# Optimization experiments

Hardware: AMD Instinct MI355X
Metric: run time of the kernel (lower is better)

Reference implementation:

```python
import jax, jax.numpy as jnp
import numpy as np
import jax.lax as lax

# ---- static config (matches init_kwargs) ----
CIN, COUT = 64, 128
KS = (3, 3, 3)
STRIDE = (1, 1, 1)
PAD = (1, 1, 1)
DIL = (1, 1, 1)
RANK, ALPHA = 16, 32.0
SCALING = ALPHA / RANK
B, D, H, W = 2, 32, 32, 32
DN = ('NCDHW', 'OIDHW', 'NCDHW')


def _out_dim(L, p, d, k, s):
    return (L + 2 * p - d * (k - 1) - 1) // s + 1


def unfold3d(x, ks, stride, pad, dil):
    """x: [B,C,D,H,W] -> [B, C*kD*kH*kW, Do, Ho, Wo], channel-major (C outer, kernel offsets inner),
    matching torch unfold ordering."""
    kD, kH, kW = ks
    sD, sH, sW = stride
    pD, pH, pW = pad
    dD, dH, dW = dil
    b, c, d_, h_, w_ = x.shape
    Do = _out_dim(d_, pD, dD, kD, sD)
    Ho = _out_dim(h_, pH, dH, kH, sH)
    Wo = _out_dim(w_, pW, dW, kW, sW)
    xp = jnp.pad(x, ((0, 0), (0, 0), (pD, pD), (pH, pH), (pW, pW)))
    slices = []
    for i in range(kD):  # fixed small loop over kernel offsets (27 iters)
        for j in range(kH):
            for l in range(kW):
                sl = xp[:, :,
                        i * dD: i * dD + (Do - 1) * sD + 1: sD,
                        j * dH: j * dH + (Ho - 1) * sH + 1: sH,
                        l * dW: l * dW + (Wo - 1) * sW + 1: sW]
                slices.append(sl)
    patches = jnp.stack(slices, axis=2)  # [B, C, K, Do, Ho, Wo]
    return patches.reshape(b, c * kD * kH * kW, Do, Ho, Wo)


def fold3d_overlap_add(grid, base_spatial, ks, stride, pad, dil):
    """Depthwise conv_transpose3d with an all-ones kernel == overlap-add fold.
    grid: [B, Cout, Do, Ho, Wo] -> [B, Cout, *base_spatial]."""
    cout = grid.shape[1]
    kern = jnp.ones((cout, 1) + ks, dtype=grid.dtype)
    pads = []
    for i in range(3):
        full = dil[i] * (ks[i] - 1)
        # torch conv_transpose out = (L-1)*s - 2p + d*(k-1) + 1 + output_padding
        opad = base_spatial[i] - ((grid.shape[2 + i] - 1) * stride[i] - 2 * pad[i] + full + 1)
        pads.append((full - pad[i], full - pad[i] + opad))
    return lax.conv_general_dilated(
        grid, kern, window_strides=(1, 1, 1), padding=pads,
        lhs_dilation=stride, rhs_dilation=dil,
        dimension_numbers=DN, feature_group_count=cout)


def setup_inputs() -> dict:
    key = jax.random.key(0)
    k1, k2, k3, k4, k5 = jax.random.split(key, 5)
    in_feat = CIN * KS[0] * KS[1] * KS[2]
    x = jax.random.normal(k1, (B, CIN, D, H, W), dtype=jnp.float32)
    weight = jax.random.normal(k2, (COUT, CIN) + KS, dtype=jnp.float32) / np.sqrt(in_feat)
    bias = jax.random.normal(k3, (COUT,), dtype=jnp.float32) * 0.01
    lora_A = jax.random.normal(k4, (RANK, in_feat), dtype=jnp.float32) / np.sqrt(in_feat)
    # torch init is zeros; use small randn so LoRA branch is numerically active
    lora_B = jax.random.normal(k5, (COUT, RANK), dtype=jnp.float32) * 0.02
    return {"x": x, "weight": weight, "bias": bias, "lora_A": lora_A, "lora_B": lora_B}


def reference(x, weight, bias, lora_A, lora_B):
    # base conv3d
    base = lax.conv_general_dilated(
        x, weight, window_strides=STRIDE, padding=[(p, p) for p in PAD],
        rhs_dilation=DIL, dimension_numbers=DN)
    base = base + bias[None, :, None, None, None]
    # im2col
    cols = unfold3d(x, KS, STRIDE, PAD, DIL)              # [B, Cin*K, Do, Ho, Wo]
    # low-rank per-patch projection: cols^T @ A^T @ B^T * scaling
    low = jnp.einsum('bkdhw,rk->brdhw', cols, lora_A)      # [B, R, Do, Ho, Wo]
    lora_grid = jnp.einsum('brdhw,or->bodhw', low, lora_B) * SCALING  # [B, Cout, ...]
    # col2im overlap-add fold back to base's spatial shape
    lora_spatial = fold3d_overlap_add(lora_grid, base.shape[2:], KS, STRIDE, PAD, DIL)
    return base + lora_spatial
```

## Files before the change

### kernel.cpp

```cpp
#include <hip/hip_runtime.h>


typedef __attribute__((ext_vector_type(8))) short short8;
typedef __attribute__((ext_vector_type(4))) float float4v;

#define PV 39304
#define PH 1156

__device__ inline unsigned short f2bf(float f) {
    unsigned int u = __float_as_uint(f);
    unsigned int r = u + 0x7FFFu + ((u >> 16) & 1u);
    return (unsigned short)(r >> 16);
}

__device__ inline void gll16(const void* g, void* l) {
    __builtin_amdgcn_global_load_lds(
        (const __attribute__((address_space(1))) unsigned int*)g,
        (__attribute__((address_space(3))) unsigned int*)l, 16, 0, 0);
}

__global__ __launch_bounds__(256) void prep_kernel(const float* __restrict__ x,
                                                   const float* __restrict__ weight,
                                                   const float* __restrict__ loraA,
                                                   unsigned short* __restrict__ xt,
                                                   unsigned short* __restrict__ wpack) {
    int t = threadIdx.x;
    int blk = blockIdx.x;
    if (blk < 1024) {
        __shared__ float tile[64][65];
        int b = blk >> 9;
        int p0 = (blk & 511) * 64;
        int d = p0 >> 10;
        int h0 = (p0 >> 5) & 31;
#pragma unroll
        for (int it = 0; it < 16; ++it) {
            int idx = it * 256 + t;
            int c = idx >> 6, pp = idx & 63;
            tile[c][pp] = x[((size_t)(b * 64 + c) << 15) + p0 + pp];
        }
        __syncthreads();
#pragma unroll
        for (int it = 0; it < 8; ++it) {
            int idx = it * 256 + t;
            int pp = idx >> 5, cp = idx & 31;
            unsigned int u0 = f2bf(tile[cp * 2][pp]);
            unsigned int u1 = f2bf(tile[cp * 2 + 1][pp]);
            int h = h0 + (pp >> 5);
            int w = pp & 31;
            size_t pidx = (size_t)((b * 34 + d + 1) * 34 + h + 1) * 34 + w + 1;
            *(unsigned int*)(xt + pidx * 64 + cp * 2) = u0 | (u1 << 16);
        }
    } else if (blk < 1332) {
        int idx = (blk - 1024) * 256 + t;
        if (idx < 78608) {
            int b = idx / PV;
            int pp = idx - b * PV;
            int d = pp / PH;
            int r2 = pp - d * PH;
            int h = r2 / 34;
            int w = r2 - h * 34;
            if (d == 0 || d == 33 || h == 0 || h == 33 || w == 0 || w == 33) {
                uint4 z = {0u, 0u, 0u, 0u};
                uint4* dst = (uint4*)(xt + (size_t)idx * 64);
#pragma unroll
                for (int i = 0; i < 8; ++i) dst[i] = z;
            }
        }
    } else {
        int gid = (blk - 1332) * 256 + t;
        if (gid < 31104) {
            int frag = gid >> 6, lane = gid & 63;
            int kb = frag / 18;
            int r18 = frag - kb * 18;
            int ks = r18 / 9;
            int nf = r18 - ks * 9;
            int l16 = lane & 15, quad = lane >> 4;
            int n = nf * 16 + l16;
            int c0 = ks * 32 + quad * 8;
            unsigned int u[4];
#pragma unroll
            for (int jp = 0; jp < 4; ++jp) {
                int ca = c0 + jp * 2, cb = ca + 1;
                float v0, v1;
                if (n < 128) {
                    v0 = weight[(n * 64 + ca) * 27 + kb];
                    v1 = weight[(n * 64 + cb) * 27 + kb];
                } else {
                    v0 = loraA[(n - 128) * 1728 + ca * 27 + kb];
                    v1 = loraA[(n - 128) * 1728 + cb * 27 + kb];
                }
                u[jp] = (unsigned)f2bf(v0) | ((unsigned)f2bf(v1) << 16);
            }
            uint4 val; val.x = u[0]; val.y = u[1]; val.z = u[2]; val.w = u[3];
            *(uint4*)(wpack + (size_t)gid * 8) = val;
        }
    }
}

__global__ __launch_bounds__(256) void gemm_kernel(const unsigned short* __restrict__ xt,
                                                   const unsigned short* __restrict__ wpack,
                                                   const float* __restrict__ bias,
                                                   float* __restrict__ out,
                                                   unsigned short* __restrict__ cbuf,
                                                   float* __restrict__ low,
                                                   int use_cbuf) {
    __shared__ unsigned short Abuf[2][9216];

    int t = threadIdx.x;
    int wv = t >> 6;
    int lane = t & 63;
    int l16 = lane & 15;
    int quad = lane >> 4;

    int bid = blockIdx.x;
    int tile = ((bid & 7) << 6) | (bid >> 3);
    int b = tile >> 8;
    int d = (tile >> 3) & 31;
    int h = ((tile & 7) << 2) + wv;

    int pbase = (((b * 34 + d) * 34 + h) * 34 + l16) * 64 + quad * 8;

    float4v acc[9][2];
#pragma unroll
    for (int nf = 0; nf < 9; ++nf)
#pragma unroll
        for (int f = 0; f < 2; ++f) acc[nf][f] = (float4v){0.f, 0.f, 0.f, 0.f};

    short8 breg[2][2][2];

    auto prefA = [&](int tap, int buf) {
        const unsigned short* src = wpack + tap * 9216;
        unsigned short* dst = &Abuf[buf][0];
#pragma unroll
        for (int j = 0; j < 4; ++j) {
            int c8 = (t + j * 256) * 8;
            gll16(src + c8, dst + c8);
        }
        if (t < 128) {
            int c8 = (t + 1024) * 8;
            gll16(src + c8, dst + c8);
        }
    };
    auto loadB = [&](int tap, int buf) {
        int ki = tap / 9;
        int kjl = tap - ki * 9;
        int kj = kjl / 3;
        int kl = kjl - kj * 3;
        int koff = ki * 73984 + kj * 2176 + kl * 64;
        const unsigned short* xp = xt + pbase + koff;
        breg[buf][0][0] = *(const short8*)(xp);
        breg[buf][0][1] = *(const short8*)(xp + 1024);
        breg[buf][1][0] = *(const short8*)(xp + 32);
        breg[buf][1][1] = *(const short8*)(xp + 1056);
    };

    prefA(0, 0);
    loadB(0, 0);
    __syncthreads();

    for (int tap = 0; tap < 27; ++tap) {
        int cur = tap & 1, nxt = cur ^ 1;
        if (tap < 26) {
            prefA(tap + 1, nxt);
            loadB(tap + 1, nxt);
        }
        const unsigned short* ab = &Abuf[cur][0] + lane * 8;
#pragma unroll
        for (int ks = 0; ks < 2; ++ks) {
            short8 af[9];
#pragma unroll
            for (int nf = 0; nf < 9; ++nf)
                af[nf] = *(const short8*)(ab + (ks * 9 + nf) * 512);
#pragma unroll
            for (int nf = 0; nf < 9; ++nf) {
                acc[nf][0] = __builtin_amdgcn_mfma_f32_16x16x32_bf16(af[nf], breg[cur][ks][0], acc[nf][0], 0, 0, 0);
                acc[nf][1] = __builtin_amdgcn_mfma_f32_16x16x32_bf16(af[nf], breg[cur][ks][1], acc[nf][1], 0, 0, 0);
            }
        }
        __syncthreads();
    }

#pragma unroll
    for (int f = 0; f < 2; ++f) {
        int w = f * 16 + l16;
        int p = d * 1024 + h * 32 + w;
#pragma unroll
        for (int nf = 0; nf < 9; ++nf) {
#pragma unroll
            for (int r = 0; r < 4; ++r) {
                int o = nf * 16 + quad * 4 + r;
                float v = acc[nf][f][r];
                if (o < 128) {
                    float c = v + bias[o];
                    if (use_cbuf) cbuf[((size_t)(b * 128 + o) << 15) + p] = f2bf(c);
                    else          out[((size_t)(b * 128 + o) << 15) + p] = c;
                } else {
                    low[((size_t)(b * 16 + (o - 128)) << 15) + p] = v;
                }
            }
        }
    }
}

__global__ __launch_bounds__(256) void foldmix_kernel(const float* __restrict__ low,
                                                      const float* __restrict__ loraB,
                                                      const unsigned short* __restrict__ cbuf,
                                                      float* __restrict__ out,
                                                      int use_cbuf) {
    __shared__ float fl[16][128];
    __shared__ float lB[2048];
    int t = threadIdx.x;
    for (int i = t; i < 2048; i += 256) lB[i] = loraB[i];

    int P0 = blockIdx.x * 128;
    int b = P0 >> 15;
    int p0 = P0 & 32767;

    {
        int pair = t & 63;
        int rg = t >> 6;
        int p = p0 + pair * 2;
        int dd0 = p >> 10, hh = (p >> 5) & 31, w0 = p & 31;
        float s[4][2];
#pragma unroll
        for (int r = 0; r < 4; ++r) { s[r][0] = 0.f; s[r][1] = 0.f; }
        const float* bb = low + ((size_t)(b * 16 + rg * 4) << 15);
        for (int dd = -1; dd <= 1; ++dd) {
            int sd = dd0 + dd;
            if ((unsigned)sd >= 32u) continue;
            for (int dh = -1; dh <= 1; ++dh) {
                int sh = hh + dh;
                if ((unsigned)sh >= 32u) continue;
                int base = (sd << 10) + (sh << 5) + w0;
#pragma unroll
                for (int r = 0; r < 4; ++r) {
                    const float* q = bb + ((size_t)r << 15) + base;
                    float vm = (w0 > 0)  ? q[-1] : 0.f;
                    float v0 = q[0], v1 = q[1];
                    float v2 = (w0 < 30) ? q[2] : 0.f;
                    s[r][0] += vm + v0 + v1;
                    s[r][1] += v0 + v1 + v2;
                }
            }
        }
#pragma unroll
        for (int r = 0; r < 4; ++r) {
            fl[rg * 4 + r][pair * 2]     = s[r][0];
            fl[rg * 4 + r][pair * 2 + 1] = s[r][1];
        }
    }
    __syncthreads();

    int wv = t >> 6;
    int lane = t & 63;
    int pl = lane * 2;
    int p = p0 + pl;
    float2 f[16];
#pragma unroll
    for (int r = 0; r < 16; ++r) f[r] = *(const float2*)&fl[r][pl];

    int o0 = wv * 32;
#pragma unroll
    for (int oi = 0; oi < 32; ++oi) {
        int o = o0 + oi;
        float sa = 0.f, sb = 0.f;
#pragma unroll
        for (int r = 0; r < 16; ++r) {
            float lw = lB[o * 16 + r];
            sa += lw * f[r].x;
            sb += lw * f[r].y;
        }
        size_t idx = ((size_t)(b * 128 + o) << 15) + p;
        float cx, cy;
        if (use_cbuf) {
            unsigned int u = *(const unsigned int*)(cbuf + idx);
            cx = __uint_as_float(u << 16);
            cy = __uint_as_float(u & 0xffff0000u);
        } else {
            float2 c = *(const float2*)(out + idx);
            cx = c.x; cy = c.y;
        }
        float2 res;
        res.x = cx + 2.0f * sa;
        res.y = cy + 2.0f * sb;
        *(float2*)(out + idx) = res;
    }
}

extern "C" void kernel_launch(void* const* d_in, const int* in_sizes, int n_in,
                              void* d_out, int out_size, void* d_ws, size_t ws_size,
                              hipStream_t stream) {
    const float* x      = (const float*)d_in[0];
    const float* weight = (const float*)d_in[1];
    const float* bias   = (const float*)d_in[2];
    const float* loraA  = (const float*)d_in[3];
    const float* loraB  = (const float*)d_in[4];
    float* out = (float*)d_out;

    char* ws = (char*)d_ws;
    unsigned short* xt    = (unsigned short*)ws;
    unsigned short* wpack = (unsigned short*)(ws + 10061824);
    float* low            = (float*)(ws + 10559488);
    unsigned short* cbuf  = (unsigned short*)(ws + 14753792);
    int use_cbuf = (ws_size >= 31531008u) ? 1 : 0;

    hipLaunchKernelGGL(prep_kernel, dim3(1454), dim3(256), 0, stream, x, weight, loraA, xt, wpack);
    hipLaunchKernelGGL(gemm_kernel, dim3(512), dim3(256), 0, stream, xt, wpack, bias, out, cbuf, low, use_cbuf);
    hipLaunchKernelGGL(foldmix_kernel, dim3(512), dim3(256), 0, stream, low, loraB, cbuf, out, use_cbuf);
}
```

Before: 147.6 us.

## Fuse prep, GEMM and fold into one persistent kernel with grid barriers

Replaces the three-kernel pipeline with a single 512-block kernel that does the bf16 prep, the implicit-GEMM conv plus LoRA projection, and the fold/mix epilogue. Phases are separated by software grid-wide barriers built on atomics. Conv accumulators stay in registers across the barrier, which removes the cbuf round trip and two kernel launches. The cost is an extra memset plus spin-wait barriers, and correctness depends on all 512 blocks being co-resident (launch bounds 256,3).

```diff
diff --git a/kernel.cpp b/kernel.cpp
--- a/kernel.cpp
+++ b/kernel.cpp
@@ -6,6 +6,7 @@
 
 #define PV 39304
 #define PH 1156
+#define NBLK 512u
 
 __device__ inline unsigned short f2bf(float f) {
     unsigned int u = __float_as_uint(f);
@@ -18,6 +19,269 @@
         (const __attribute__((address_space(1))) unsigned int*)g,
         (__attribute__((address_space(3))) unsigned int*)l, 16, 0, 0);
 }
+
+__device__ inline void grid_barrier(unsigned int* bar, int slot) {
+    __syncthreads();
+    if (threadIdx.x == 0) {
+        __threadfence();
+        unsigned int* c = bar + slot * 32;
+        atomicAdd(c, 1u);
+        while (__hip_atomic_load(c, __ATOMIC_ACQUIRE, __HIP_MEMORY_SCOPE_AGENT) < NBLK) {
+            __builtin_amdgcn_s_sleep(2);
+        }
+    }
+    __syncthreads();
+    __threadfence();
+}
+
+__global__ __launch_bounds__(256, 3) void fused_kernel(
+    const float* __restrict__ x, const float* __restrict__ weight,
+    const float* __restrict__ bias, const float* __restrict__ loraA,
+    const float* __restrict__ loraB, float* __restrict__ out,
+    unsigned short* __restrict__ xt, unsigned short* __restrict__ wpack,
+    float* __restrict__ low, unsigned int* __restrict__ bar)
+{
+    __shared__ __align__(16) char smraw[36864];
+    int t = threadIdx.x;
+    int bid = blockIdx.x;
+
+    {
+        float (*tile)[65] = (float (*)[65])smraw;
+        for (int u = bid; u < 1454; u += 512) {
+            if (u < 1024) {
+                int pb = u >> 9;
+                int p0 = (u & 511) * 64;
+                int pd = p0 >> 10;
+                int ph0 = (p0 >> 5) & 31;
+#pragma unroll
+                for (int it = 0; it < 16; ++it) {
+                    int idx = it * 256 + t;
+                    int c = idx >> 6, pp = idx & 63;
+                    tile[c][pp] = x[((size_t)(pb * 64 + c) << 15) + p0 + pp];
+                }
+                __syncthreads();
+#pragma unroll
+                for (int it = 0; it < 8; ++it) {
+                    int idx = it * 256 + t;
+                    int pp = idx >> 5, cp = idx & 31;
+                    unsigned int u0 = f2bf(tile[cp * 2][pp]);
+                    unsigned int u1 = f2bf(tile[cp * 2 + 1][pp]);
+                    int ph = ph0 + (pp >> 5);
+                    int pw = pp & 31;
+                    size_t pidx = (size_t)((pb * 34 + pd + 1) * 34 + ph + 1) * 34 + pw + 1;
+                    *(unsigned int*)(xt + pidx * 64 + cp * 2) = u0 | (u1 << 16);
+                }
+            } else if (u < 1332) {
+                int idx = (u - 1024) * 256 + t;
+                if (idx < 78608) {
+                    int pb = idx / PV;
+                    int pp = idx - pb * PV;
+                    int pd = pp / PH;
+                    int r2 = pp - pd * PH;
+                    int ph = r2 / 34;
+                    int pw = r2 - ph * 34;
+                    if (pd == 0 || pd == 33 || ph == 0 || ph == 33 || pw == 0 || pw == 33) {
+                        uint4 z = {0u, 0u, 0u, 0u};
+                        uint4* dst = (uint4*)(xt + (size_t)idx * 64);
+#pragma unroll
+                        for (int i = 0; i < 8; ++i) dst[i] = z;
+                    }
+                }
+            } else {
+                int gid = (u - 1332) * 256 + t;
+                if (gid < 31104) {
+                    int frag = gid >> 6, ln = gid & 63;
+                    int kb = frag / 18;
+                    int r18 = frag - kb * 18;
+                    int ks = r18 / 9;
+                    int nf = r18 - ks * 9;
+                    int pl16 = ln & 15, pq = ln >> 4;
+                    int n = nf * 16 + pl16;
+                    int c0 = ks * 32 + pq * 8;
+                    unsigned int uu[4];
+#pragma unroll
+                    for (int jp = 0; jp < 4; ++jp) {
+                        int ca = c0 + jp * 2, cb = ca + 1;
+                        float v0, v1;
+                        if (n < 128) {
+                            v0 = weight[(n * 64 + ca) * 27 + kb];
+                            v1 = weight[(n * 64 + cb) * 27 + kb];
+                        } else {
+                            v0 = loraA[(n - 128) * 1728 + ca * 27 + kb];
+                            v1 = loraA[(n - 128) * 1728 + cb * 27 + kb];
+                        }
+                        uu[jp] = (unsigned)f2bf(v0) | ((unsigned)f2bf(v1) << 16);
+                    }
+                    uint4 val; val.x = uu[0]; val.y = uu[1]; val.z = uu[2]; val.w = uu[3];
+                    *(uint4*)(wpack + (size_t)gid * 8) = val;
+                }
+            }
+            __syncthreads();
+        }
+    }
+
+    grid_barrier(bar, 0);
+
+    int wv = t >> 6;
+    int lane = t & 63;
+    int l16 = lane & 15;
+    int quad = lane >> 4;
+
+    int tl = ((bid & 7) << 6) | (bid >> 3);
+    int b = tl >> 8;
+    int d = (tl >> 3) & 31;
+    int hb = (tl & 7) << 2;
+    int h = hb + wv;
+
+    unsigned short (*Abuf)[9216] = (unsigned short (*)[9216])smraw;
+
+    int pbase = (((b * 34 + d) * 34 + h) * 34 + l16) * 64 + quad * 8;
+
+    float4v acc[9][2];
+#pragma unroll
+    for (int nf = 0; nf < 9; ++nf)
+#pragma unroll
+        for (int f = 0; f < 2; ++f) acc[nf][f] = (float4v){0.f, 0.f, 0.f, 0.f};
+
+    short8 breg[2][2][2];
+
+    auto prefA = [&](int tap, int buf) {
+        const unsigned short* src = wpack + tap * 9216;
+        unsigned short* dst = &Abuf[buf][0];
+#pragma unroll
+        for (int j = 0; j < 4; ++j) {
+            int c8 = (t + j * 256) * 8;
+            gll16(src + c8, dst + c8);
+        }
+        if (t < 128) {
+            int c8 = (t + 1024) * 8;
+            gll16(src + c8, dst + c8);
+        }
+    };
+    auto loadB = [&](int tap, int buf) {
+        int ki = tap / 9;
+        int kjl = tap - ki * 9;
+        int kj = kjl / 3;
+        int kl = kjl - kj * 3;
+        int koff = ki * 73984 + kj * 2176 + kl * 64;
+        const unsigned short* xp = xt + pbase + koff;
+        breg[buf][0][0] = *(const short8*)(xp);
+        breg[buf][0][1] = *(const short8*)(xp + 1024);
+        breg[buf][1][0] = *(const short8*)(xp + 32);
+        breg[buf][1][1] = *(const short8*)(xp + 1056);
+    };
+
+    prefA(0, 0);
+    loadB(0, 0);
+    __syncthreads();
+
+    for (int tap = 0; tap < 27; ++tap) {
+        int cur = tap & 1, nxt = cur ^ 1;
+        if (tap < 26) {
+            prefA(tap + 1, nxt);
+            loadB(tap + 1, nxt);
+        }
+        const unsigned short* ab = &Abuf[cur][0] + lane * 8;
+#pragma unroll
+        for (int ks = 0; ks < 2; ++ks) {
+            short8 af[9];
+#pragma unroll
+            for (int nf = 0; nf < 9; ++nf)
+                af[nf] = *(const short8*)(ab + (ks * 9 + nf) * 512);
+#pragma unroll
+            for (int nf = 0; nf < 9; ++nf) {
+                acc[nf][0] = __builtin_amdgcn_mfma_f32_16x16x32_bf16(af[nf], breg[cur][ks][0], acc[nf][0], 0, 0, 0);
+                acc[nf][1] = __builtin_amdgcn_mfma_f32_16x16x32_bf16(af[nf], breg[cur][ks][1], acc[nf][1], 0, 0, 0);
+            }
+        }
+        __syncthreads();
+    }
+
+    {
+        int p = d * 1024 + h * 32;
+#pragma unroll
+        for (int f = 0; f < 2; ++f)
+#pragma unroll
+            for (int r = 0; r < 4; ++r)
+                low[((size_t)(b * 16 + quad * 4 + r) << 15) + p + f * 16 + l16] = acc[8][f][r];
+    }
+
+    grid_barrier(bar, 1);
+
+    {
+        float* fl  = (float*)smraw;
+        float* lBp = (float*)(smraw + 8192);
+        float* bsh = (float*)(smraw + 16384);
+
+        for (int i = t; i < 2048; i += 256) {
+            int o = i & 127, rr = i >> 7;
+            lBp[rr * 128 + o] = 2.0f * loraB[o * 16 + rr];
+        }
+        if (t < 128) bsh[t] = bias[t];
+
+        {
+            int pair = t & 63, rg = t >> 6;
+            int lp = pair * 2;
+            int hh = hb + (lp >> 5);
+            int w0 = lp & 31;
+            float s0[4], s1[4];
+#pragma unroll
+            for (int r = 0; r < 4; ++r) { s0[r] = 0.f; s1[r] = 0.f; }
+            const float* bb = low + ((size_t)(b * 16 + rg * 4) << 15);
+            for (int dd = -1; dd <= 1; ++dd) {
+                int sd = d + dd;
+                if ((unsigned)sd >= 32u) continue;
+                for (int dh = -1; dh <= 1; ++dh) {
+                    int sh = hh + dh;
+                    if ((unsigned)sh >= 32u) continue;
+                    int base = (sd << 10) + (sh << 5) + w0;
+#pragma unroll
+                    for (int r = 0; r < 4; ++r) {
+                        const float* q = bb + ((size_t)r << 15) + base;
+                        float vm = (w0 > 0)  ? q[-1] : 0.f;
+                        float v0 = q[0], v1 = q[1];
+                        float v2 = (w0 < 30) ? q[2] : 0.f;
+                        s0[r] += vm + v0 + v1;
+                        s1[r] += v0 + v1 + v2;
+                    }
+                }
+            }
+#pragma unroll
+            for (int r = 0; r < 4; ++r) {
+                fl[(rg * 4 + r) * 128 + lp]     = s0[r];
+                fl[(rg * 4 + r) * 128 + lp + 1] = s1[r];
+            }
+        }
+        __syncthreads();
+
+        float fa[16], fb[16];
+        int base0 = wv * 32 + l16;
+#pragma unroll
+        for (int rr = 0; rr < 16; ++rr) {
+            fa[rr] = fl[rr * 128 + base0];
+            fb[rr] = fl[rr * 128 + base0 + 16];
+        }
+#pragma unroll
+        for (int nf = 0; nf < 8; ++nf) {
+            float4v sv0 = (float4v){0.f, 0.f, 0.f, 0.f};
+            float4v sv1 = (float4v){0.f, 0.f, 0.f, 0.f};
+#pragma unroll
+            for (int rr = 0; rr < 16; ++rr) {
+                float4v lw = *(const float4v*)&lBp[rr * 128 + nf * 16 + quad * 4];
+                sv0 += lw * fa[rr];
+                sv1 += lw * fb[rr];
+            }
+            size_t ob0 = ((size_t)(b * 128 + nf * 16 + quad * 4) << 15) + (size_t)(d * 1024 + h * 32);
+#pragma unroll
+            for (int r = 0; r < 4; ++r) {
+                float bv = bsh[nf * 16 + quad * 4 + r];
+                out[ob0 + ((size_t)r << 15) + l16]      = acc[nf][0][r] + bv + sv0[r];
+                out[ob0 + ((size_t)r << 15) + 16 + l16] = acc[nf][1][r] + bv + sv1[r];
+            }
+        }
+    }
+}
+
 
 __global__ __launch_bounds__(256) void prep_kernel(const float* __restrict__ x,
                                                    const float* __restrict__ weight,
@@ -301,10 +565,17 @@
     unsigned short* xt    = (unsigned short*)ws;
     unsigned short* wpack = (unsigned short*)(ws + 10061824);
     float* low            = (float*)(ws + 10559488);
+    unsigned int* bar     = (unsigned int*)(ws + 14753792);
     unsigned short* cbuf  = (unsigned short*)(ws + 14753792);
-    int use_cbuf = (ws_size >= 31531008u) ? 1 : 0;
-
-    hipLaunchKernelGGL(prep_kernel, dim3(1454), dim3(256), 0, stream, x, weight, loraA, xt, wpack);
-    hipLaunchKernelGGL(gemm_kernel, dim3(512), dim3(256), 0, stream, xt, wpack, bias, out, cbuf, low, use_cbuf);
-    hipLaunchKernelGGL(foldmix_kernel, dim3(512), dim3(256), 0, stream, low, loraB, cbuf, out, use_cbuf);
-}
+
+    if (ws_size >= 14754048u) {
+        hipMemsetAsync(bar, 0, 256, stream);
+        hipLaunchKernelGGL(fused_kernel, dim3(512), dim3(256), 0, stream,
+                           x, weight, bias, loraA, loraB, out, xt, wpack, low, bar);
+    } else {
+        int use_cbuf = (ws_size >= 31531008u) ? 1 : 0;
+        hipLaunchKernelGGL(prep_kernel, dim3(1454), dim3(256), 0, stream, x, weight, loraA, xt, wpack);
+        hipLaunchKernelGGL(gemm_kernel, dim3(512), dim3(256), 0, stream, xt, wpack, bias, out, cbuf, low, use_cbuf);
+        hipLaunchKernelGGL(foldmix_kernel, dim3(512), dim3(256), 0, stream, low, loraB, cbuf, out, use_cbuf);
+    }
+}
```

After: 327.2 us. 122% more time.

## Load GEMM weight fragments directly from global memory instead of LDS double buffer

Applied to the files above, without the earlier changes.

Removes the LDS double-buffered staging of packed weights (global_load_lds plus a per-tap barrier). Each wave now reads its weight fragments straight from global memory, where they should be served from L2/L1 because every block shares them. The change also drops the explicit software prefetch of B and sets launch bounds to request two blocks per CU. The risks are repeated global/L1 traffic for the weights, since all four waves load the same fragments, and exposed load latency now that nothing is prefetched.

```diff
diff --git a/kernel.cpp b/kernel.cpp
--- a/kernel.cpp
+++ b/kernel.cpp
@@ -11,12 +11,6 @@
     unsigned int u = __float_as_uint(f);
     unsigned int r = u + 0x7FFFu + ((u >> 16) & 1u);
     return (unsigned short)(r >> 16);
-}
-
-__device__ inline void gll16(const void* g, void* l) {
-    __builtin_amdgcn_global_load_lds(
-        (const __attribute__((address_space(1))) unsigned int*)g,
-        (__attribute__((address_space(3))) unsigned int*)l, 16, 0, 0);
 }
 
 __global__ __launch_bounds__(256) void prep_kernel(const float* __restrict__ x,
@@ -97,15 +91,13 @@
     }
 }
 
-__global__ __launch_bounds__(256) void gemm_kernel(const unsigned short* __restrict__ xt,
-                                                   const unsigned short* __restrict__ wpack,
-                                                   const float* __restrict__ bias,
-                                                   float* __restrict__ out,
-                                                   unsigned short* __restrict__ cbuf,
-                                                   float* __restrict__ low,
-                                                   int use_cbuf) {
-    __shared__ unsigned short Abuf[2][9216];
-
+__global__ __launch_bounds__(256, 2) void gemm_kernel(const unsigned short* __restrict__ xt,
+                                                      const unsigned short* __restrict__ wpack,
+                                                      const float* __restrict__ bias,
+                                                      float* __restrict__ out,
+                                                      unsigned short* __restrict__ cbuf,
+                                                      float* __restrict__ low,
+                                                      int use_cbuf) {
     int t = threadIdx.x;
     int wv = t >> 6;
     int lane = t & 63;
@@ -119,6 +111,7 @@
     int h = ((tile & 7) << 2) + wv;
 
     int pbase = (((b * 34 + d) * 34 + h) * 34 + l16) * 64 + quad * 8;
+    const unsigned short* ap = wpack + lane * 8;
 
     float4v acc[9][2];
 #pragma unroll
@@ -126,58 +119,37 @@
 #pragma unroll
         for (int f = 0; f < 2; ++f) acc[nf][f] = (float4v){0.f, 0.f, 0.f, 0.f};
 
-    short8 breg[2][2][2];
-
-    auto prefA = [&](int tap, int buf) {
-        const unsigned short* src = wpack + tap * 9216;
-        unsigned short* dst = &Abuf[buf][0];
-#pragma unroll
-        for (int j = 0; j < 4; ++j) {
-            int c8 = (t + j * 256) * 8;
-            gll16(src + c8, dst + c8);
-        }
-        if (t < 128) {
-            int c8 = (t + 1024) * 8;
-            gll16(src + c8, dst + c8);
-        }
-    };
-    auto loadB = [&](int tap, int buf) {
+    for (int tap = 0; tap < 27; ++tap) {
         int ki = tap / 9;
         int kjl = tap - ki * 9;
         int kj = kjl / 3;
         int kl = kjl - kj * 3;
         int koff = ki * 73984 + kj * 2176 + kl * 64;
         const unsigned short* xp = xt + pbase + koff;
-        breg[buf][0][0] = *(const short8*)(xp);
-        breg[buf][0][1] = *(const short8*)(xp + 1024);
-        breg[buf][1][0] = *(const short8*)(xp + 32);
-        breg[buf][1][1] = *(const short8*)(xp + 1056);
-    };
-
-    prefA(0, 0);
-    loadB(0, 0);
-    __syncthreads();
-
-    for (int tap = 0; tap < 27; ++tap) {
-        int cur = tap & 1, nxt = cur ^ 1;
-        if (tap < 26) {
-            prefA(tap + 1, nxt);
-            loadB(tap + 1, nxt);
-        }
-        const unsigned short* ab = &Abuf[cur][0] + lane * 8;
-#pragma unroll
-        for (int ks = 0; ks < 2; ++ks) {
-            short8 af[9];
+
+        short8 b00 = *(const short8*)(xp);
+        short8 b01 = *(const short8*)(xp + 1024);
+        short8 b10 = *(const short8*)(xp + 32);
+        short8 b11 = *(const short8*)(xp + 1056);
+
+        const unsigned short* at = ap + tap * 9216;
+        short8 af[2][9];
+#pragma unroll
+        for (int ks = 0; ks < 2; ++ks)
 #pragma unroll
             for (int nf = 0; nf < 9; ++nf)
-                af[nf] = *(const short8*)(ab + (ks * 9 + nf) * 512);
-#pragma unroll
-            for (int nf = 0; nf < 9; ++nf) {
-                acc[nf][0] = __builtin_amdgcn_mfma_f32_16x16x32_bf16(af[nf], breg[cur][ks][0], acc[nf][0], 0, 0, 0);
-                acc[nf][1] = __builtin_amdgcn_mfma_f32_16x16x32_bf16(af[nf], breg[cur][ks][1], acc[nf][1], 0, 0, 0);
-            }
-        }
-        __syncthreads();
+                af[ks][nf] = *(const short8*)(at + (ks * 9 + nf) * 512);
+
+#pragma unroll
+        for (int nf = 0; nf < 9; ++nf) {
+            acc[nf][0] = __builtin_amdgcn_mfma_f32_16x16x32_bf16(af[0][nf], b00, acc[nf][0], 0, 0, 0);
+            acc[nf][1] = __builtin_amdgcn_mfma_f32_16x16x32_bf16(af[0][nf], b01, acc[nf][1], 0, 0, 0);
+        }
+#pragma unroll
+        for (int nf = 0; nf < 9; ++nf) {
+            acc[nf][0] = __builtin_amdgcn_mfma_f32_16x16x32_bf16(af[1][nf], b10, acc[nf][0], 0, 0, 0);
+            acc[nf][1] = __builtin_amdgcn_mfma_f32_16x16x32_bf16(af[1][nf], b11, acc[nf][1], 0, 0, 0);
+        }
     }
 
 #pragma unroll
```

Result: slower. 202.6 us (+37.2%).

## Process two taps per pipeline stage to halve barriers in implicit GEMM

Applied to the files above, without the earlier changes.

Restructures the 27-tap main loop so each double-buffered stage loads and computes two kernel taps at once. LDS weight buffers are doubled to hold two taps, and B fragments for two taps sit in registers. The last tap is handled in a tail. This halves the number of __syncthreads and issues larger prefetch batches. In exchange it doubles LDS use (about 72KB) and raises register pressure, which may lower occupancy.

```diff
diff --git a/kernel.cpp b/kernel.cpp
--- a/kernel.cpp
+++ b/kernel.cpp
@@ -104,7 +104,7 @@
                                                    unsigned short* __restrict__ cbuf,
                                                    float* __restrict__ low,
                                                    int use_cbuf) {
-    __shared__ unsigned short Abuf[2][9216];
+    __shared__ unsigned short Abuf[2][18432];
 
     int t = threadIdx.x;
     int wv = t >> 6;
@@ -126,10 +126,20 @@
 #pragma unroll
         for (int f = 0; f < 2; ++f) acc[nf][f] = (float4v){0.f, 0.f, 0.f, 0.f};
 
-    short8 breg[2][2][2];
-
-    auto prefA = [&](int tap, int buf) {
-        const unsigned short* src = wpack + tap * 9216;
+    short8 G0a[2][2], G0b[2][2];
+    short8 G1a[2][2], G1b[2][2];
+
+    auto prefAg = [&](int g, int buf) {
+        const unsigned short* src = wpack + g * 18432;
+        unsigned short* dst = &Abuf[buf][0];
+#pragma unroll
+        for (int j = 0; j < 9; ++j) {
+            int c8 = (t + j * 256) * 8;
+            gll16(src + c8, dst + c8);
+        }
+    };
+    auto prefA1 = [&](int buf) {
+        const unsigned short* src = wpack + 26 * 9216;
         unsigned short* dst = &Abuf[buf][0];
 #pragma unroll
         for (int j = 0; j < 4; ++j) {
@@ -141,30 +151,20 @@
             gll16(src + c8, dst + c8);
         }
     };
-    auto loadB = [&](int tap, int buf) {
+    auto loadB1 = [&](int tap, short8 (&br)[2][2]) {
         int ki = tap / 9;
         int kjl = tap - ki * 9;
         int kj = kjl / 3;
         int kl = kjl - kj * 3;
         int koff = ki * 73984 + kj * 2176 + kl * 64;
         const unsigned short* xp = xt + pbase + koff;
-        breg[buf][0][0] = *(const short8*)(xp);
-        breg[buf][0][1] = *(const short8*)(xp + 1024);
-        breg[buf][1][0] = *(const short8*)(xp + 32);
-        breg[buf][1][1] = *(const short8*)(xp + 1056);
+        br[0][0] = *(const short8*)(xp);
+        br[0][1] = *(const short8*)(xp + 1024);
+        br[1][0] = *(const short8*)(xp + 32);
+        br[1][1] = *(const short8*)(xp + 1056);
     };
-
-    prefA(0, 0);
-    loadB(0, 0);
-    __syncthreads();
-
-    for (int tap = 0; tap < 27; ++tap) {
-        int cur = tap & 1, nxt = cur ^ 1;
-        if (tap < 26) {
-            prefA(tap + 1, nxt);
-            loadB(tap + 1, nxt);
-        }
-        const unsigned short* ab = &Abuf[cur][0] + lane * 8;
+    auto compute1 = [&](const unsigned short* abase, const short8 (&br)[2][2]) {
+        const unsigned short* ab = abase + lane * 8;
 #pragma unroll
         for (int ks = 0; ks < 2; ++ks) {
             short8 af[9];
@@ -173,12 +173,38 @@
                 af[nf] = *(const short8*)(ab + (ks * 9 + nf) * 512);
 #pragma unroll
             for (int nf = 0; nf < 9; ++nf) {
-                acc[nf][0] = __builtin_amdgcn_mfma_f32_16x16x32_bf16(af[nf], breg[cur][ks][0], acc[nf][0], 0, 0, 0);
-                acc[nf][1] = __builtin_amdgcn_mfma_f32_16x16x32_bf16(af[nf], breg[cur][ks][1], acc[nf][1], 0, 0, 0);
-            }
-        }
+                acc[nf][0] = __builtin_amdgcn_mfma_f32_16x16x32_bf16(af[nf], br[ks][0], acc[nf][0], 0, 0, 0);
+                acc[nf][1] = __builtin_amdgcn_mfma_f32_16x16x32_bf16(af[nf], br[ks][1], acc[nf][1], 0, 0, 0);
+            }
+        }
+    };
+
+    prefAg(0, 0);
+    loadB1(0, G0a);
+    loadB1(1, G0b);
+    __syncthreads();
+
+    for (int tt = 0; tt < 6; ++tt) {
+        int g = 2 * tt;
+        prefAg(g + 1, 1);
+        loadB1(2 * (g + 1), G1a);
+        loadB1(2 * (g + 1) + 1, G1b);
+        compute1(&Abuf[0][0], G0a);
+        compute1(&Abuf[0][0] + 9216, G0b);
         __syncthreads();
-    }
+        prefAg(g + 2, 0);
+        loadB1(2 * (g + 2), G0a);
+        loadB1(2 * (g + 2) + 1, G0b);
+        compute1(&Abuf[1][0], G1a);
+        compute1(&Abuf[1][0] + 9216, G1b);
+        __syncthreads();
+    }
+    prefA1(1);
+    loadB1(26, G1a);
+    compute1(&Abuf[0][0], G0a);
+    compute1(&Abuf[0][0] + 9216, G0b);
+    __syncthreads();
+    compute1(&Abuf[1][0], G1a);
 
 #pragma unroll
     for (int f = 0; f < 2; ++f) {
```

Measured after the change: 173.2 us. +17.3%, slower.
